# Kernel optimization log

Hardware: AMD Instinct MI355X
Metric: run time of the kernel (lower is better)

Reference implementation:

```python
import jax, jax.numpy as jnp
import numpy as np

P = 7
SCALE = 1.0 / 16.0
PRE_NMS, POST_NMS, NMS_TH, MIN_SIZE = 6000, 300, 0.7, 16.0


def _generate_anchors(base_size=16, ratios=(0.5, 1.0, 2.0), scales=(8, 16, 32)):
    ratios = np.array(ratios, dtype=np.float64)
    scales = np.array(scales, dtype=np.float64)
    base = np.array([0, 0, base_size - 1, base_size - 1], dtype=np.float64)

    def whctrs(a):
        w = a[2] - a[0] + 1
        h = a[3] - a[1] + 1
        return w, h, a[0] + 0.5 * (w - 1), a[1] + 0.5 * (h - 1)

    def mk(ws, hs, xc, yc):
        return np.stack([xc - 0.5 * (ws - 1), yc - 0.5 * (hs - 1),
                         xc + 0.5 * (ws - 1), yc + 0.5 * (hs - 1)], axis=1)

    w, h, xc, yc = whctrs(base)
    size = w * h
    ws = np.round(np.sqrt(size / ratios))
    hs = np.round(ws * ratios)
    ratio_anchors = mk(ws, hs, xc, yc)
    outs = []
    for ra in ratio_anchors:
        w, h, xc, yc = whctrs(ra)
        outs.append(mk(w * scales, h * scales, xc, yc))
    return np.vstack(outs).astype(np.float32)  # [9,4]


def _conv(x, w, b, relu=True):
    y = jax.lax.conv_general_dilated(x, w, (1, 1), 'SAME',
                                     dimension_numbers=('NCHW', 'OIHW', 'NCHW'))
    y = y + b[None, :, None, None]
    return jnp.maximum(y, 0.0) if relu else y


def _maxpool(x):
    return jax.lax.reduce_window(x, -jnp.inf, jax.lax.max,
                                 (1, 1, 2, 2), (1, 1, 2, 2), 'VALID')


def _vgg(x, ws, bs):
    i = 0
    for nb, n in enumerate((2, 2, 3, 3, 3)):
        for _ in range(n):
            x = _conv(x, ws[i], bs[i])
            i += 1
        if nb < 4:
            x = _maxpool(x)
    return x  # conv5_3, stride 16, 512 ch


def _decode(anchors, deltas):
    w = anchors[:, 2] - anchors[:, 0] + 1.0
    h = anchors[:, 3] - anchors[:, 1] + 1.0
    cx = anchors[:, 0] + 0.5 * w
    cy = anchors[:, 1] + 0.5 * h
    pcx = deltas[:, 0] * w + cx
    pcy = deltas[:, 1] * h + cy
    pw = jnp.exp(deltas[:, 2]) * w
    ph = jnp.exp(deltas[:, 3]) * h
    return jnp.stack([pcx - 0.5 * pw, pcy - 0.5 * ph,
                      pcx + 0.5 * pw, pcy + 0.5 * ph], axis=1)


def _nms_keep(boxes, thresh):
    x1, y1, x2, y2 = boxes[:, 0], boxes[:, 1], boxes[:, 2], boxes[:, 3]
    areas = (x2 - x1 + 1.0) * (y2 - y1 + 1.0)
    xx1 = jnp.maximum(x1[:, None], x1[None, :])
    yy1 = jnp.maximum(y1[:, None], y1[None, :])
    xx2 = jnp.minimum(x2[:, None], x2[None, :])
    yy2 = jnp.minimum(y2[:, None], y2[None, :])
    inter = jnp.maximum(xx2 - xx1 + 1.0, 0.0) * jnp.maximum(yy2 - yy1 + 1.0, 0.0)
    iou = inter / (areas[:, None] + areas[None, :] - inter)
    n = boxes.shape[0]
    idx = jnp.arange(n)

    def body(i, keep):
        sup = (iou[i] > thresh) & (idx > i) & keep[i]
        return keep & (~sup)

    return jax.lax.fori_loop(0, n, body, jnp.ones(n, dtype=bool))


def _proposals(prob_fg, bbox_deltas, im_info):
    _, _, H, W = prob_fg.shape
    shift_x = np.arange(W) * 16.0
    shift_y = np.arange(H) * 16.0
    sx, sy = np.meshgrid(shift_x, shift_y)
    shifts = np.stack([sx.ravel(), sy.ravel(), sx.ravel(), sy.ravel()], axis=1).astype(np.float32)
    anchors = jnp.asarray((_generate_anchors()[None, :, :] + shifts[:, None, :]).reshape(-1, 4))
    scores = prob_fg.transpose(0, 2, 3, 1).reshape(-1)
    deltas = bbox_deltas.transpose(0, 2, 3, 1).reshape(-1, 4)
    boxes = _decode(anchors, deltas)
    boxes = jnp.stack([jnp.clip(boxes[:, 0], 0.0, im_info[1] - 1.0),
                       jnp.clip(boxes[:, 1], 0.0, im_info[0] - 1.0),
                       jnp.clip(boxes[:, 2], 0.0, im_info[1] - 1.0),
                       jnp.clip(boxes[:, 3], 0.0, im_info[0] - 1.0)], axis=1)
    ws = boxes[:, 2] - boxes[:, 0] + 1.0
    hs = boxes[:, 3] - boxes[:, 1] + 1.0
    ms = MIN_SIZE * im_info[2]
    scores = jnp.where((ws >= ms) & (hs >= ms), scores, -jnp.inf)
    k = min(PRE_NMS, int(scores.shape[0]))
    top_s, order = jax.lax.top_k(scores, k)
    tb = boxes[order]
    keep = _nms_keep(tb, NMS_TH)
    prio = jnp.where(keep, jnp.arange(k), k)
    sel = jnp.argsort(prio)[:POST_NMS]
    ob = tb[sel]
    rois = jnp.concatenate([jnp.zeros((POST_NMS, 1), ob.dtype), ob], axis=1)
    # original proposal layer runs in numpy -> detached from the graph
    return jax.lax.stop_gradient(rois)


def _roi_pool(feat, rois):
    f = feat[0]  # [C,Hf,Wf]
    C, Hf, Wf = f.shape
    hh = jnp.arange(Hf)
    ww = jnp.arange(Wf)
    pb = jnp.arange(P)

    def one(roi):
        x1 = jnp.round(roi[1] * SCALE).astype(jnp.int32)
        y1 = jnp.round(roi[2] * SCALE).astype(jnp.int32)
        x2 = jnp.round(roi[3] * SCALE).astype(jnp.int32)
        y2 = jnp.round(roi[4] * SCALE).astype(jnp.int32)
        rh = jnp.maximum(y2 - y1 + 1, 1).astype(f.dtype)
        rw = jnp.maximum(x2 - x1 + 1, 1).astype(f.dtype)
        bh = rh / P
        bw = rw / P
        hs_ = jnp.clip(jnp.floor(pb * bh).astype(jnp.int32) + y1, 0, Hf)
        he_ = jnp.clip(jnp.ceil((pb + 1) * bh).astype(jnp.int32) + y1, 0, Hf)
        ws_ = jnp.clip(jnp.floor(pb * bw).astype(jnp.int32) + x1, 0, Wf)
        we_ = jnp.clip(jnp.ceil((pb + 1) * bw).astype(jnp.int32) + x1, 0, Wf)
        mh = (hh[None, :] >= hs_[:, None]) & (hh[None, :] < he_[:, None])  # [P,Hf]
        mw = (ww[None, :] >= ws_[:, None]) & (ww[None, :] < we_[:, None])  # [P,Wf]
        t = jnp.where(mw[:, None, None, :], f[None], -jnp.inf).max(axis=-1)   # [Ppw,C,Hf]
        v = jnp.where(mh[:, None, None, :], t[None], -jnp.inf).max(axis=-1)   # [Pph,Ppw,C]
        v = jnp.where(jnp.isfinite(v), v, 0.0)  # empty bins -> 0
        return jnp.transpose(v, (2, 0, 1))  # [C,P,P]

    return jax.lax.map(one, rois)  # [N,C,P,P]


def _forward(im_data, im_info, vws, vbs, rpn_w, rpn_b, score_w, score_b,
             bbox_w, bbox_b, fc6_w, fc6_b, fc7_w, fc7_b, cls_w, cls_b, breg_w, breg_b):
    x = jnp.transpose(im_data, (0, 3, 1, 2))
    feat = _vgg(x, vws, vbs)
    r = _conv(feat, rpn_w, rpn_b, relu=True)
    score = _conv(r, score_w, score_b, relu=False)  # [1,18,H,W]
    bd = _conv(r, bbox_w, bbox_b, relu=False)       # [1,36,H,W]
    _, _, H, W = score.shape
    # reshape_layer to (1,2,9H,W) + softmax over dim1 == softmax over (1,2,9,H,W) axis 1
    prob = jax.nn.softmax(score.reshape(1, 2, 9, H, W), axis=1).reshape(1, 18, H, W)
    prob_fg = prob[:, 9:, :, :]
    rois = _proposals(prob_fg, bd, im_info)
    pooled = _roi_pool(feat, rois).reshape(POST_NMS, -1)  # [300, 512*7*7]
    h6 = jnp.maximum(pooled @ fc6_w.T + fc6_b, 0.0)
    h7 = jnp.maximum(h6 @ fc7_w.T + fc7_b, 0.0)
    cls_score = h7 @ cls_w.T + cls_b
    cls_prob = jax.nn.softmax(cls_score, axis=-1)
    bbox_pred = h7 @ breg_w.T + breg_b
    return cls_prob, bbox_pred, rois


def setup_inputs() -> dict:
    key = jax.random.key(0)
    ks = iter(jax.random.split(key, 64))
    cfg = [(3, 64), (64, 64), (64, 128), (128, 128), (128, 256), (256, 256), (256, 256),
           (256, 512), (512, 512), (512, 512), (512, 512), (512, 512), (512, 512)]
    inp = {}
    inp['im_data'] = jax.random.uniform(next(ks), (1, 600, 1000, 3), jnp.float32) * 255.0 - 122.0
    inp['im_info'] = jnp.array([600.0, 1000.0, 1.0], jnp.float32)
    for i, (ci, co) in enumerate(cfg, start=1):
        std = float(np.sqrt(2.0 / (ci * 9)))
        inp['vw%d' % i] = jax.random.normal(next(ks), (co, ci, 3, 3), jnp.float32) * std
        inp['vb%d' % i] = jnp.zeros((co,), jnp.float32)
    inp['rpn_w'] = jax.random.normal(next(ks), (512, 512, 3, 3), jnp.float32) * float(np.sqrt(2.0 / (512 * 9)))
    inp['rpn_b'] = jnp.zeros((512,), jnp.float32)
    inp['score_w'] = jax.random.normal(next(ks), (18, 512, 1, 1), jnp.float32) * 0.01
    inp['score_b'] = jnp.zeros((18,), jnp.float32)
    inp['bbox_w'] = jax.random.normal(next(ks), (36, 512, 1, 1), jnp.float32) * 0.01
    inp['bbox_b'] = jnp.zeros((36,), jnp.float32)
    inp['fc6_w'] = jax.random.normal(next(ks), (4096, 512 * 7 * 7), jnp.float32) * 0.005
    inp['fc6_b'] = jnp.zeros((4096,), jnp.float32)
    inp['fc7_w'] = jax.random.normal(next(ks), (4096, 4096), jnp.float32) * 0.01
    inp['fc7_b'] = jnp.zeros((4096,), jnp.float32)
    inp['cls_w'] = jax.random.normal(next(ks), (21, 4096), jnp.float32) * 0.01
    inp['cls_b'] = jnp.zeros((21,), jnp.float32)
    inp['breg_w'] = jax.random.normal(next(ks), (84, 4096), jnp.float32) * 0.001
    inp['breg_b'] = jnp.zeros((84,), jnp.float32)
    return inp


def reference(im_data, im_info, vw1, vb1, vw2, vb2, vw3, vb3, vw4, vb4, vw5, vb5,
              vw6, vb6, vw7, vb7, vw8, vb8, vw9, vb9, vw10, vb10, vw11, vb11,
              vw12, vb12, vw13, vb13, rpn_w, rpn_b, score_w, score_b, bbox_w, bbox_b,
              fc6_w, fc6_b, fc7_w, fc7_b, cls_w, cls_b, breg_w, breg_b):
    vws = [vw1, vw2, vw3, vw4, vw5, vw6, vw7, vw8, vw9, vw10, vw11, vw12, vw13]
    vbs = [vb1, vb2, vb3, vb4, vb5, vb6, vb7, vb8, vb9, vb10, vb11, vb12, vb13]
    return _forward(im_data, im_info, vws, vbs, rpn_w, rpn_b, score_w, score_b,
                    bbox_w, bbox_b, fc6_w, fc6_b, fc7_w, fc7_b, cls_w, cls_b, breg_w, breg_b)
```

## Files before the change

### kernel.cpp

```cpp
#include <hip/hip_runtime.h>
#include <math.h>


#define NPOS 2294
#define FH 37
#define FW 62
#define NANCH 20646
#define NSORT 32768
#define PRE_NMS 6000
#define POST_NMS 300
#define NWORD 94

__device__ const float ANCHORS[9][4] = {
    {-84.f,  -40.f,   99.f,  55.f},
    {-176.f, -88.f,  191.f, 103.f},
    {-360.f, -184.f, 375.f, 199.f},
    {-56.f,  -56.f,   71.f,  71.f},
    {-120.f, -120.f, 135.f, 135.f},
    {-248.f, -248.f, 263.f, 263.f},
    {-36.f,  -80.f,   51.f,  95.f},
    {-80.f,  -168.f,  95.f, 183.f},
    {-168.f, -344.f, 183.f, 359.f},
};

__global__ __launch_bounds__(256) void conv3x3(
    const float* __restrict__ in, const float* __restrict__ w,
    const float* __restrict__ bias, float* __restrict__ out,
    int C, int H, int W, int relu, int nhwc)
{
    __shared__ float patch[10 * 34];
    const int tx = threadIdx.x, ty = threadIdx.y;
    const int tid = ty * 32 + tx;
    const int x0 = blockIdx.x * 32, y0 = blockIdx.y * 8;
    const int k0 = blockIdx.z * 8;
    const size_t HW = (size_t)H * W;

    float acc[8];
#pragma unroll
    for (int i = 0; i < 8; ++i) acc[i] = 0.f;

    for (int c = 0; c < C; ++c) {
        __syncthreads();
#pragma unroll
        for (int l = 0; l < 2; ++l) {
            int idx = tid + l * 256;
            if (idx < 340) {
                int py = idx / 34, px = idx - py * 34;
                int gy = y0 + py - 1, gx = x0 + px - 1;
                float v = 0.f;
                if (gy >= 0 && gy < H && gx >= 0 && gx < W)
                    v = nhwc ? in[((size_t)gy * W + gx) * C + c]
                             : in[(size_t)c * HW + (size_t)gy * W + gx];
                patch[idx] = v;
            }
        }
        __syncthreads();
        float r0 = patch[(ty + 0) * 34 + tx + 0];
        float r1 = patch[(ty + 0) * 34 + tx + 1];
        float r2 = patch[(ty + 0) * 34 + tx + 2];
        float r3 = patch[(ty + 1) * 34 + tx + 0];
        float r4 = patch[(ty + 1) * 34 + tx + 1];
        float r5 = patch[(ty + 1) * 34 + tx + 2];
        float r6 = patch[(ty + 2) * 34 + tx + 0];
        float r7 = patch[(ty + 2) * 34 + tx + 1];
        float r8 = patch[(ty + 2) * 34 + tx + 2];
        const float* wp = w + ((size_t)k0 * C + c) * 9;
#pragma unroll
        for (int ko = 0; ko < 8; ++ko) {
            const float* wk = wp + (size_t)ko * C * 9;
            acc[ko] += wk[0] * r0 + wk[1] * r1 + wk[2] * r2
                     + wk[3] * r3 + wk[4] * r4 + wk[5] * r5
                     + wk[6] * r6 + wk[7] * r7 + wk[8] * r8;
        }
    }

    int gx = x0 + tx, gy = y0 + ty;
    if (gx < W && gy < H) {
#pragma unroll
        for (int ko = 0; ko < 8; ++ko) {
            float v = acc[ko] + bias[k0 + ko];
            if (relu) v = fmaxf(v, 0.f);
            out[(size_t)(k0 + ko) * HW + (size_t)gy * W + gx] = v;
        }
    }
}

__global__ void maxpool2(const float* __restrict__ in, float* __restrict__ out,
                         int C, int H, int W)
{
    int Ho = H >> 1, Wo = W >> 1;
    int total = C * Ho * Wo;
    int idx = blockIdx.x * blockDim.x + threadIdx.x;
    if (idx >= total) return;
    int c = idx / (Ho * Wo);
    int r = idx - c * (Ho * Wo);
    int y = r / Wo, x = r - y * Wo;
    const float* p = in + (size_t)c * H * W + (size_t)(2 * y) * W + 2 * x;
    out[idx] = fmaxf(fmaxf(p[0], p[1]), fmaxf(p[W], p[W + 1]));
}

__global__ void conv1x1(const float* __restrict__ in, const float* __restrict__ w,
                        const float* __restrict__ b, float* __restrict__ out,
                        int C, int P, int K)
{
    int p = blockIdx.x * blockDim.x + threadIdx.x;
    int k = blockIdx.y;
    if (p >= P || k >= K) return;
    const float* wr = w + (size_t)k * C;
    float acc = b[k];
    for (int c = 0; c < C; ++c) acc += wr[c] * in[(size_t)c * P + p];
    out[(size_t)k * P + p] = acc;
}

__global__ void decode_anchors(const float* __restrict__ score,
                               const float* __restrict__ bbox,
                               const float* __restrict__ iminfo,
                               float* __restrict__ boxes,
                               unsigned long long* __restrict__ keys)
{
    int idx = blockIdx.x * blockDim.x + threadIdx.x;
    if (idx >= NSORT) return;
    if (idx >= NANCH) { keys[idx] = ~0ULL; return; }
    int p = idx / 9, a = idx - p * 9;
    int y = p / FW, x = p - y * FW;

    float s0 = score[a * NPOS + p], s1 = score[(9 + a) * NPOS + p];
    float mx = fmaxf(s0, s1);
    float e0 = expf(s0 - mx), e1 = expf(s1 - mx);
    float prob = e1 / (e0 + e1);

    float ax1 = ANCHORS[a][0] + 16.f * x;
    float ay1 = ANCHORS[a][1] + 16.f * y;
    float ax2 = ANCHORS[a][2] + 16.f * x;
    float ay2 = ANCHORS[a][3] + 16.f * y;
    float aw = ax2 - ax1 + 1.f, ah = ay2 - ay1 + 1.f;
    float cx = ax1 + 0.5f * aw, cy = ay1 + 0.5f * ah;

    float d0 = bbox[(4 * a + 0) * NPOS + p];
    float d1 = bbox[(4 * a + 1) * NPOS + p];
    float d2 = bbox[(4 * a + 2) * NPOS + p];
    float d3 = bbox[(4 * a + 3) * NPOS + p];
    float pcx = d0 * aw + cx, pcy = d1 * ah + cy;
    float pw = expf(d2) * aw, ph = expf(d3) * ah;

    float imh = iminfo[0], imw = iminfo[1], sc = iminfo[2];
    float x1 = fminf(fmaxf(pcx - 0.5f * pw, 0.f), imw - 1.f);
    float y1 = fminf(fmaxf(pcy - 0.5f * ph, 0.f), imh - 1.f);
    float x2 = fminf(fmaxf(pcx + 0.5f * pw, 0.f), imw - 1.f);
    float y2 = fminf(fmaxf(pcy + 0.5f * ph, 0.f), imh - 1.f);
    boxes[idx * 4 + 0] = x1; boxes[idx * 4 + 1] = y1;
    boxes[idx * 4 + 2] = x2; boxes[idx * 4 + 3] = y2;

    float wsz = x2 - x1 + 1.f, hsz = y2 - y1 + 1.f;
    float ms = 16.f * sc;
    float s = (wsz >= ms && hsz >= ms) ? prob : -INFINITY;
    unsigned u = __float_as_uint(s);
    u = (u & 0x80000000u) ? ~u : (u | 0x80000000u);
    unsigned k32 = ~u;
    keys[idx] = ((unsigned long long)k32 << 32) | (unsigned)idx;
}

__global__ void bitonic_step(unsigned long long* __restrict__ keys, int j, int k)
{
    int i = blockIdx.x * blockDim.x + threadIdx.x;
    int ixj = i ^ j;
    if (ixj > i && ixj < NSORT) {
        unsigned long long a = keys[i], b = keys[ixj];
        bool up = ((i & k) == 0);
        if ((a > b) == up) { keys[i] = b; keys[ixj] = a; }
    }
}

__global__ void gather_top(const unsigned long long* __restrict__ keys,
                           const float* __restrict__ boxes, float* __restrict__ tb)
{
    int r = blockIdx.x * blockDim.x + threadIdx.x;
    if (r >= PRE_NMS) return;
    int idx = (int)(keys[r] & 0xffffffffULL);
    ((float4*)tb)[r] = ((const float4*)boxes)[idx];
}

__global__ __launch_bounds__(128) void iou_sup(const float* __restrict__ tb,
                                               unsigned long long* __restrict__ sup)
{
    int i = blockIdx.x;
    int wj = threadIdx.x;
    if (wj >= NWORD) return;
    float4 bi = ((const float4*)tb)[i];
    float ai = (bi.z - bi.x + 1.f) * (bi.w - bi.y + 1.f);
    unsigned long long m = 0;
    int jbase = wj * 64;
    for (int b = 0; b < 64; ++b) {
        int j = jbase + b;
        if (j <= i || j >= PRE_NMS) continue;
        float4 bj = ((const float4*)tb)[j];
        float xx1 = fmaxf(bi.x, bj.x), yy1 = fmaxf(bi.y, bj.y);
        float xx2 = fminf(bi.z, bj.z), yy2 = fminf(bi.w, bj.w);
        float iw = fmaxf(xx2 - xx1 + 1.f, 0.f), ih = fmaxf(yy2 - yy1 + 1.f, 0.f);
        float inter = iw * ih;
        float aj = (bj.z - bj.x + 1.f) * (bj.w - bj.y + 1.f);
        float iou = inter / (ai + aj - inter);
        if (iou > 0.7f) m |= (1ULL << b);
    }
    sup[(size_t)i * NWORD + wj] = m;
}

__global__ __launch_bounds__(128) void nms_seq(const unsigned long long* __restrict__ sup,
                                               unsigned long long* __restrict__ keepg)
{
    __shared__ unsigned long long keep[NWORD];
    int t = threadIdx.x;
    if (t < NWORD) keep[t] = ~0ULL;
    __syncthreads();
    for (int i = 0; i < PRE_NMS; ++i) {
        bool k = (keep[i >> 6] >> (i & 63)) & 1ULL;
        __syncthreads();
        if (k && t < NWORD) keep[t] &= ~sup[(size_t)i * NWORD + t];
        __syncthreads();
    }
    if (t < NWORD) keepg[t] = keep[t];
}

__global__ void select_rois(const unsigned long long* __restrict__ keepg,
                            const float* __restrict__ tb,
                            float* __restrict__ rois, float* __restrict__ out_rois)
{
    if (threadIdx.x != 0 || blockIdx.x != 0) return;
    int cnt = 0;
    for (int pass = 0; pass < 2 && cnt < POST_NMS; ++pass) {
        for (int i = 0; i < PRE_NMS && cnt < POST_NMS; ++i) {
            bool k = (keepg[i >> 6] >> (i & 63)) & 1ULL;
            if ((pass == 0) == k) {
                float v0 = 0.f;
                float v1 = tb[i * 4 + 0], v2 = tb[i * 4 + 1];
                float v3 = tb[i * 4 + 2], v4 = tb[i * 4 + 3];
                rois[cnt * 5 + 0] = v0; rois[cnt * 5 + 1] = v1; rois[cnt * 5 + 2] = v2;
                rois[cnt * 5 + 3] = v3; rois[cnt * 5 + 4] = v4;
                out_rois[cnt * 5 + 0] = v0; out_rois[cnt * 5 + 1] = v1; out_rois[cnt * 5 + 2] = v2;
                out_rois[cnt * 5 + 3] = v3; out_rois[cnt * 5 + 4] = v4;
                ++cnt;
            }
        }
    }
}

__global__ __launch_bounds__(256) void roi_pool(const float* __restrict__ feat,
                                                const float* __restrict__ rois,
                                                float* __restrict__ pooled)
{
    int b = blockIdx.x;
    const float* r = rois + b * 5;
    int x1 = (int)rintf(r[1] * 0.0625f);
    int y1 = (int)rintf(r[2] * 0.0625f);
    int x2 = (int)rintf(r[3] * 0.0625f);
    int y2 = (int)rintf(r[4] * 0.0625f);
    float bh = (float)max(y2 - y1 + 1, 1) / 7.f;
    float bw = (float)max(x2 - x1 + 1, 1) / 7.f;
    for (int o = threadIdx.x; o < 512 * 49; o += 256) {
        int c = o / 49, rem = o - c * 49;
        int ph = rem / 7, pw = rem - ph * 7;
        int hs = min(max((int)floorf(ph * bh) + y1, 0), FH);
        int he = min(max((int)ceilf((ph + 1) * bh) + y1, 0), FH);
        int wst = min(max((int)floorf(pw * bw) + x1, 0), FW);
        int wen = min(max((int)ceilf((pw + 1) * bw) + x1, 0), FW);
        float m = -INFINITY;
        for (int yy = hs; yy < he; ++yy)
            for (int xx = wst; xx < wen; ++xx)
                m = fmaxf(m, feat[c * NPOS + yy * FW + xx]);
        pooled[(size_t)b * 25088 + o] = (he > hs && wen > wst) ? m : 0.f;
    }
}

__global__ __launch_bounds__(256) void gemm_nt(const float* __restrict__ A,
                                               const float* __restrict__ Wt,
                                               const float* __restrict__ bias,
                                               float* __restrict__ out,
                                               int M, int N, int K, int relu)
{
    __shared__ float Ws[32 * 260];
    __shared__ float As[32 * 20];
    int t = threadIdx.x;
    int n0 = blockIdx.x * 256, m0 = blockIdx.y * 16;
    int tnn = t & 63, tmm = t >> 6;
    float acc[4][4];
#pragma unroll
    for (int i = 0; i < 4; ++i)
#pragma unroll
        for (int j = 0; j < 4; ++j) acc[i][j] = 0.f;

    for (int k0 = 0; k0 < K; k0 += 32) {
        __syncthreads();
        {
            const float4* wr = (const float4*)(Wt + (size_t)(n0 + t) * K + k0);
#pragma unroll
            for (int q = 0; q < 8; ++q) {
                float4 v = wr[q];
                Ws[(4 * q + 0) * 260 + t] = v.x;
                Ws[(4 * q + 1) * 260 + t] = v.y;
                Ws[(4 * q + 2) * 260 + t] = v.z;
                Ws[(4 * q + 3) * 260 + t] = v.w;
            }
        }
        if (t < 128) {
            int m = t >> 3, q = t & 7;
            float4 v = make_float4(0.f, 0.f, 0.f, 0.f);
            if (m0 + m < M) v = *(const float4*)(A + (size_t)(m0 + m) * K + k0 + 4 * q);
            As[(4 * q + 0) * 20 + m] = v.x;
            As[(4 * q + 1) * 20 + m] = v.y;
            As[(4 * q + 2) * 20 + m] = v.z;
            As[(4 * q + 3) * 20 + m] = v.w;
        }
        __syncthreads();
#pragma unroll 8
        for (int kk = 0; kk < 32; ++kk) {
            float4 wv = *(const float4*)&Ws[kk * 260 + tnn * 4];
            float4 av = *(const float4*)&As[kk * 20 + tmm * 4];
            acc[0][0] += av.x * wv.x; acc[0][1] += av.x * wv.y;
            acc[0][2] += av.x * wv.z; acc[0][3] += av.x * wv.w;
            acc[1][0] += av.y * wv.x; acc[1][1] += av.y * wv.y;
            acc[1][2] += av.y * wv.z; acc[1][3] += av.y * wv.w;
            acc[2][0] += av.z * wv.x; acc[2][1] += av.z * wv.y;
            acc[2][2] += av.z * wv.z; acc[2][3] += av.z * wv.w;
            acc[3][0] += av.w * wv.x; acc[3][1] += av.w * wv.y;
            acc[3][2] += av.w * wv.z; acc[3][3] += av.w * wv.w;
        }
    }
    int n = n0 + tnn * 4;
    float4 bv = *(const float4*)(bias + n);
#pragma unroll
    for (int i = 0; i < 4; ++i) {
        int m = m0 + tmm * 4 + i;
        if (m < M) {
            float4 o;
            o.x = acc[i][0] + bv.x; o.y = acc[i][1] + bv.y;
            o.z = acc[i][2] + bv.z; o.w = acc[i][3] + bv.w;
            if (relu) {
                o.x = fmaxf(o.x, 0.f); o.y = fmaxf(o.y, 0.f);
                o.z = fmaxf(o.z, 0.f); o.w = fmaxf(o.w, 0.f);
            }
            *(float4*)(out + (size_t)m * N + n) = o;
        }
    }
}

__global__ void fc_small(const float* __restrict__ A, const float* __restrict__ Wt,
                         const float* __restrict__ bias, float* __restrict__ out,
                         int N, int K)
{
    int m = blockIdx.x, n = threadIdx.x;
    if (n >= N) return;
    const float4* a = (const float4*)(A + (size_t)m * K);
    const float4* w = (const float4*)(Wt + (size_t)n * K);
    float acc = bias[n];
    for (int q = 0; q < K / 4; ++q) {
        float4 av = a[q], wv = w[q];
        acc += av.x * wv.x + av.y * wv.y + av.z * wv.z + av.w * wv.w;
    }
    out[(size_t)m * N + n] = acc;
}

__global__ void softmax21(const float* __restrict__ in, float* __restrict__ out)
{
    int r = blockIdx.x * blockDim.x + threadIdx.x;
    if (r >= POST_NMS) return;
    const float* x = in + r * 21;
    float m = x[0];
    for (int j = 1; j < 21; ++j) m = fmaxf(m, x[j]);
    float e[21], s = 0.f;
    for (int j = 0; j < 21; ++j) { e[j] = expf(x[j] - m); s += e[j]; }
    float inv = 1.f / s;
    for (int j = 0; j < 21; ++j) out[r * 21 + j] = e[j] * inv;
}

extern "C" void kernel_launch(void* const* d_in, const int* in_sizes, int n_in,
                              void* d_out, int out_size, void* d_ws, size_t ws_size,
                              hipStream_t stream)
{
    const float* im_data = (const float*)d_in[0];
    const float* im_info = (const float*)d_in[1];
    const float* vw[13]; const float* vb[13];
    for (int i = 0; i < 13; ++i) { vw[i] = (const float*)d_in[2 + 2 * i]; vb[i] = (const float*)d_in[3 + 2 * i]; }
    const float* rpn_w   = (const float*)d_in[28];
    const float* rpn_b   = (const float*)d_in[29];
    const float* score_w = (const float*)d_in[30];
    const float* score_b = (const float*)d_in[31];
    const float* bbox_w  = (const float*)d_in[32];
    const float* bbox_b  = (const float*)d_in[33];
    const float* fc6_w   = (const float*)d_in[34];
    const float* fc6_b   = (const float*)d_in[35];
    const float* fc7_w   = (const float*)d_in[36];
    const float* fc7_b   = (const float*)d_in[37];
    const float* cls_w   = (const float*)d_in[38];
    const float* cls_b   = (const float*)d_in[39];
    const float* breg_w  = (const float*)d_in[40];
    const float* breg_b  = (const float*)d_in[41];

    float* ws = (float*)d_ws;
    const size_t oA    = 0;
    const size_t oB    = 38400000;
    const size_t oF    = 76800000;
    const size_t oRPN  = oF    + 1174528;
    const size_t oSC   = oRPN  + 1174528;
    const size_t oBB   = oSC   + 41292;
    const size_t oBOX  = oBB   + 82584;
    const size_t oKEY  = oBOX  + 82584;
    const size_t oTB   = oKEY  + 65536;
    const size_t oSUP  = oTB   + 24000;
    const size_t oKEEP = oSUP  + 1128000;
    const size_t oROI  = oKEEP + 256;
    const size_t oPOOL = oROI  + 1536;
    const size_t oH6   = oPOOL + 7526400;
    const size_t oH7   = oH6   + 1228800;
    const size_t oCLS  = oH7   + 1228800;

    float* bufA = ws + oA;
    float* bufB = ws + oB;
    float* feat = ws + oF;
    float* rpn  = ws + oRPN;
    float* scr  = ws + oSC;
    float* bbx  = ws + oBB;
    float* boxes = ws + oBOX;
    unsigned long long* keys = (unsigned long long*)(ws + oKEY);
    float* tb = ws + oTB;
    unsigned long long* sup = (unsigned long long*)(ws + oSUP);
    unsigned long long* keepg = (unsigned long long*)(ws + oKEEP);
    float* rois = ws + oROI;
    float* pooled = ws + oPOOL;
    float* h6 = ws + oH6;
    float* h7 = ws + oH7;
    float* clsb = ws + oCLS;

    float* out = (float*)d_out;
    float* out_bbox = out + 6300;
    float* out_rois = out + 31500;

    dim3 cblk(32, 8);
    auto conv = [&](const float* in, const float* w, const float* b, float* o,
                    int C, int H, int W, int K, int relu, int nhwc) {
        dim3 grid((W + 31) / 32, (H + 7) / 8, K / 8);
        conv3x3<<<grid, cblk, 0, stream>>>(in, w, b, o, C, H, W, relu, nhwc);
    };
    auto pool = [&](const float* in, float* o, int C, int H, int W) {
        int total = C * (H / 2) * (W / 2);
        maxpool2<<<(total + 255) / 256, 256, 0, stream>>>(in, o, C, H, W);
    };

    conv(im_data, vw[0], vb[0], bufA, 3, 600, 1000, 64, 1, 1);
    conv(bufA, vw[1], vb[1], bufB, 64, 600, 1000, 64, 1, 0);
    pool(bufB, bufA, 64, 600, 1000);
    conv(bufA, vw[2], vb[2], bufB, 64, 300, 500, 128, 1, 0);
    conv(bufB, vw[3], vb[3], bufA, 128, 300, 500, 128, 1, 0);
    pool(bufA, bufB, 128, 300, 500);
    conv(bufB, vw[4], vb[4], bufA, 128, 150, 250, 256, 1, 0);
    conv(bufA, vw[5], vb[5], bufB, 256, 150, 250, 256, 1, 0);
    conv(bufB, vw[6], vb[6], bufA, 256, 150, 250, 256, 1, 0);
    pool(bufA, bufB, 256, 150, 250);
    conv(bufB, vw[7], vb[7], bufA, 256, 75, 125, 512, 1, 0);
    conv(bufA, vw[8], vb[8], bufB, 512, 75, 125, 512, 1, 0);
    conv(bufB, vw[9], vb[9], bufA, 512, 75, 125, 512, 1, 0);
    pool(bufA, bufB, 512, 75, 125);
    conv(bufB, vw[10], vb[10], bufA, 512, FH, FW, 512, 1, 0);
    conv(bufA, vw[11], vb[11], bufB, 512, FH, FW, 512, 1, 0);
    conv(bufB, vw[12], vb[12], feat, 512, FH, FW, 512, 1, 0);

    conv(feat, rpn_w, rpn_b, rpn, 512, FH, FW, 512, 1, 0);
    {
        dim3 g((NPOS + 255) / 256, 18);
        conv1x1<<<g, 256, 0, stream>>>(rpn, score_w, score_b, scr, 512, NPOS, 18);
    }
    {
        dim3 g((NPOS + 255) / 256, 36);
        conv1x1<<<g, 256, 0, stream>>>(rpn, bbox_w, bbox_b, bbx, 512, NPOS, 36);
    }

    decode_anchors<<<NSORT / 256, 256, 0, stream>>>(scr, bbx, im_info, boxes, keys);
    for (int k = 2; k <= NSORT; k <<= 1)
        for (int j = k >> 1; j > 0; j >>= 1)
            bitonic_step<<<NSORT / 256, 256, 0, stream>>>(keys, j, k);
    gather_top<<<(PRE_NMS + 255) / 256, 256, 0, stream>>>(keys, boxes, tb);
    iou_sup<<<PRE_NMS, 128, 0, stream>>>(tb, sup);
    nms_seq<<<1, 128, 0, stream>>>(sup, keepg);
    select_rois<<<1, 64, 0, stream>>>(keepg, tb, rois, out_rois);

    roi_pool<<<POST_NMS, 256, 0, stream>>>(feat, rois, pooled);
    {
        dim3 g(4096 / 256, (POST_NMS + 15) / 16);
        gemm_nt<<<g, 256, 0, stream>>>(pooled, fc6_w, fc6_b, h6, POST_NMS, 4096, 25088, 1);
        gemm_nt<<<g, 256, 0, stream>>>(h6, fc7_w, fc7_b, h7, POST_NMS, 4096, 4096, 1);
    }
    fc_small<<<POST_NMS, 96, 0, stream>>>(h7, cls_w, cls_b, clsb, 21, 4096);
    fc_small<<<POST_NMS, 96, 0, stream>>>(h7, breg_w, breg_b, out_bbox, 84, 4096);
    softmax21<<<(POST_NMS + 255) / 256, 256, 0, stream>>>(clsb, out);
    (void)in_sizes; (void)n_in; (void)out_size; (void)ws_size;
}
```

Measured before the change: 17.50 ms.

## Batch conv channels, shared-memory bitonic sort, wave NMS, split-K FC GEMMs

Result: slower. 20.00 ms (+14.3%).

```diff
diff --git a/kernel.cpp b/kernel.cpp
--- a/kernel.cpp
+++ b/kernel.cpp
@@ -10,6 +10,7 @@
 #define PRE_NMS 6000
 #define POST_NMS 300
 #define NWORD 94
+#define GS 8
 
 __device__ const float ANCHORS[9][4] = {
     {-84.f,  -40.f,   99.f,  55.f},
@@ -28,7 +29,7 @@
     const float* __restrict__ bias, float* __restrict__ out,
     int C, int H, int W, int relu, int nhwc)
 {
-    __shared__ float patch[10 * 34];
+    __shared__ float patch[4][10][34];
     const int tx = threadIdx.x, ty = threadIdx.y;
     const int tid = ty * 32 + tx;
     const int x0 = blockIdx.x * 32, y0 = blockIdx.y * 8;
@@ -39,38 +40,49 @@
 #pragma unroll
     for (int i = 0; i < 8; ++i) acc[i] = 0.f;
 
-    for (int c = 0; c < C; ++c) {
+    for (int c0 = 0; c0 < C; c0 += 4) {
+        const int nc = (C - c0 >= 4) ? 4 : (C - c0);
         __syncthreads();
-#pragma unroll
-        for (int l = 0; l < 2; ++l) {
-            int idx = tid + l * 256;
-            if (idx < 340) {
-                int py = idx / 34, px = idx - py * 34;
-                int gy = y0 + py - 1, gx = x0 + px - 1;
-                float v = 0.f;
-                if (gy >= 0 && gy < H && gx >= 0 && gx < W)
-                    v = nhwc ? in[((size_t)gy * W + gx) * C + c]
-                             : in[(size_t)c * HW + (size_t)gy * W + gx];
-                patch[idx] = v;
+        for (int idx = tid; idx < nc * 340; idx += 256) {
+            int cc = idx / 340, rr = idx - cc * 340;
+            int py = rr / 34, px = rr - py * 34;
+            int gy = y0 + py - 1, gx = x0 + px - 1;
+            float v = 0.f;
+            if (gy >= 0 && gy < H && gx >= 0 && gx < W)
+                v = nhwc ? in[((size_t)gy * W + gx) * C + (c0 + cc)]
+                         : in[(size_t)(c0 + cc) * HW + (size_t)gy * W + gx];
+            patch[cc][py][px] = v;
+        }
+        __syncthreads();
+        if (nc == 4) {
+#pragma unroll
+            for (int cc = 0; cc < 4; ++cc) {
+                float r0 = patch[cc][ty][tx],     r1 = patch[cc][ty][tx + 1],     r2 = patch[cc][ty][tx + 2];
+                float r3 = patch[cc][ty + 1][tx], r4 = patch[cc][ty + 1][tx + 1], r5 = patch[cc][ty + 1][tx + 2];
+                float r6 = patch[cc][ty + 2][tx], r7 = patch[cc][ty + 2][tx + 1], r8 = patch[cc][ty + 2][tx + 2];
+                const float* wp = w + ((size_t)k0 * C + (c0 + cc)) * 9;
+#pragma unroll
+                for (int ko = 0; ko < 8; ++ko) {
+                    const float* wk = wp + (size_t)ko * C * 9;
+                    acc[ko] += wk[0] * r0 + wk[1] * r1 + wk[2] * r2
+                             + wk[3] * r3 + wk[4] * r4 + wk[5] * r5
+                             + wk[6] * r6 + wk[7] * r7 + wk[8] * r8;
+                }
             }
-        }
-        __syncthreads();
-        float r0 = patch[(ty + 0) * 34 + tx + 0];
-        float r1 = patch[(ty + 0) * 34 + tx + 1];
-        float r2 = patch[(ty + 0) * 34 + tx + 2];
-        float r3 = patch[(ty + 1) * 34 + tx + 0];
-        float r4 = patch[(ty + 1) * 34 + tx + 1];
-        float r5 = patch[(ty + 1) * 34 + tx + 2];
-        float r6 = patch[(ty + 2) * 34 + tx + 0];
-        float r7 = patch[(ty + 2) * 34 + tx + 1];
-        float r8 = patch[(ty + 2) * 34 + tx + 2];
-        const float* wp = w + ((size_t)k0 * C + c) * 9;
-#pragma unroll
-        for (int ko = 0; ko < 8; ++ko) {
-            const float* wk = wp + (size_t)ko * C * 9;
-            acc[ko] += wk[0] * r0 + wk[1] * r1 + wk[2] * r2
-                     + wk[3] * r3 + wk[4] * r4 + wk[5] * r5
-                     + wk[6] * r6 + wk[7] * r7 + wk[8] * r8;
+        } else {
+            for (int cc = 0; cc < nc; ++cc) {
+                float r0 = patch[cc][ty][tx],     r1 = patch[cc][ty][tx + 1],     r2 = patch[cc][ty][tx + 2];
+                float r3 = patch[cc][ty + 1][tx], r4 = patch[cc][ty + 1][tx + 1], r5 = patch[cc][ty + 1][tx + 2];
+                float r6 = patch[cc][ty + 2][tx], r7 = patch[cc][ty + 2][tx + 1], r8 = patch[cc][ty + 2][tx + 2];
+                const float* wp = w + ((size_t)k0 * C + (c0 + cc)) * 9;
+#pragma unroll
+                for (int ko = 0; ko < 8; ++ko) {
+                    const float* wk = wp + (size_t)ko * C * 9;
+                    acc[ko] += wk[0] * r0 + wk[1] * r1 + wk[2] * r2
+                             + wk[3] * r3 + wk[4] * r4 + wk[5] * r5
+                             + wk[6] * r6 + wk[7] * r7 + wk[8] * r8;
+                }
+            }
         }
     }
 
@@ -169,6 +181,40 @@
         bool up = ((i & k) == 0);
         if ((a > b) == up) { keys[i] = b; keys[ixj] = a; }
     }
+}
+
+__global__ __launch_bounds__(1024) void bitonic_local(unsigned long long* __restrict__ keys,
+                                                      int mode, int kbig)
+{
+    __shared__ unsigned long long s[2048];
+    const int t = threadIdx.x;
+    const int base = blockIdx.x * 2048;
+    s[t] = keys[base + t];
+    s[t + 1024] = keys[base + t + 1024];
+    __syncthreads();
+    if (mode == 0) {
+        for (int k = 2; k <= 2048; k <<= 1) {
+            for (int j = k >> 1; j > 0; j >>= 1) {
+                int i = ((t & ~(j - 1)) << 1) | (t & (j - 1));
+                int ixj = i + j;
+                bool up = (((base + i) & k) == 0);
+                unsigned long long a = s[i], b = s[ixj];
+                if ((a > b) == up) { s[i] = b; s[ixj] = a; }
+                __syncthreads();
+            }
+        }
+    } else {
+        for (int j = 1024; j > 0; j >>= 1) {
+            int i = ((t & ~(j - 1)) << 1) | (t & (j - 1));
+            int ixj = i + j;
+            bool up = (((base + i) & kbig) == 0);
+            unsigned long long a = s[i], b = s[ixj];
+            if ((a > b) == up) { s[i] = b; s[ixj] = a; }
+            __syncthreads();
+        }
+    }
+    keys[base + t] = s[t];
+    keys[base + t + 1024] = s[t + 1024];
 }
 
 __global__ void gather_top(const unsigned long long* __restrict__ keys,
@@ -205,41 +251,65 @@
     sup[(size_t)i * NWORD + wj] = m;
 }
 
-__global__ __launch_bounds__(128) void nms_seq(const unsigned long long* __restrict__ sup,
-                                               unsigned long long* __restrict__ keepg)
-{
-    __shared__ unsigned long long keep[NWORD];
-    int t = threadIdx.x;
-    if (t < NWORD) keep[t] = ~0ULL;
+__global__ void nms_wave(const unsigned long long* __restrict__ sup,
+                         unsigned long long* __restrict__ keepg)
+{
+    const int l = threadIdx.x;
+    const bool hi = (64 + l < NWORD);
+    unsigned long long w0 = ~0ULL;
+    unsigned long long w1 = hi ? ~0ULL : 0ULL;
+
+    unsigned long long a0, b0, a1, b1, a2, b2, a3, b3, a4, b4, a5, b5, a6, b6, a7, b7;
+#define LOADROW(A, B, r) do { \
+        A = sup[(size_t)(r) * NWORD + l]; \
+        B = hi ? sup[(size_t)(r) * NWORD + 64 + l] : 0ULL; } while (0)
+    LOADROW(a0, b0, 0); LOADROW(a1, b1, 1); LOADROW(a2, b2, 2); LOADROW(a3, b3, 3);
+    LOADROW(a4, b4, 4); LOADROW(a5, b5, 5); LOADROW(a6, b6, 6); LOADROW(a7, b7, 7);
+
+    for (int g = 0; g < PRE_NMS; g += 8) {
+#define STEP(A, B, ii) do { \
+        int i = g + (ii); \
+        int wi = i >> 6; \
+        unsigned long long kw = (wi < 64) ? __shfl(w0, wi) : __shfl(w1, wi - 64); \
+        if ((kw >> (i & 63)) & 1ULL) { w0 &= ~(A); w1 &= ~(B); } \
+        int nr = i + 8; \
+        if (nr < PRE_NMS) LOADROW(A, B, nr); } while (0)
+        STEP(a0, b0, 0); STEP(a1, b1, 1); STEP(a2, b2, 2); STEP(a3, b3, 3);
+        STEP(a4, b4, 4); STEP(a5, b5, 5); STEP(a6, b6, 6); STEP(a7, b7, 7);
+#undef STEP
+    }
+#undef LOADROW
+    if (l == 29) w1 &= (1ULL << 48) - 1ULL;
+    keepg[l] = w0;
+    if (hi) keepg[64 + l] = w1;
+}
+
+__global__ __launch_bounds__(128) void select_rois(
+    const unsigned long long* __restrict__ keepg,
+    const float* __restrict__ tb,
+    float* __restrict__ rois, float* __restrict__ out_rois)
+{
+    __shared__ int wbase[NWORD + 1];
+    const int t = threadIdx.x;
+    if (t == 0) {
+        int s = 0;
+        for (int w = 0; w < NWORD; ++w) { wbase[w] = s; s += __popcll(keepg[w]); }
+        wbase[NWORD] = s;
+    }
     __syncthreads();
-    for (int i = 0; i < PRE_NMS; ++i) {
-        bool k = (keep[i >> 6] >> (i & 63)) & 1ULL;
-        __syncthreads();
-        if (k && t < NWORD) keep[t] &= ~sup[(size_t)i * NWORD + t];
-        __syncthreads();
-    }
-    if (t < NWORD) keepg[t] = keep[t];
-}
-
-__global__ void select_rois(const unsigned long long* __restrict__ keepg,
-                            const float* __restrict__ tb,
-                            float* __restrict__ rois, float* __restrict__ out_rois)
-{
-    if (threadIdx.x != 0 || blockIdx.x != 0) return;
-    int cnt = 0;
-    for (int pass = 0; pass < 2 && cnt < POST_NMS; ++pass) {
-        for (int i = 0; i < PRE_NMS && cnt < POST_NMS; ++i) {
-            bool k = (keepg[i >> 6] >> (i & 63)) & 1ULL;
-            if ((pass == 0) == k) {
-                float v0 = 0.f;
-                float v1 = tb[i * 4 + 0], v2 = tb[i * 4 + 1];
-                float v3 = tb[i * 4 + 2], v4 = tb[i * 4 + 3];
-                rois[cnt * 5 + 0] = v0; rois[cnt * 5 + 1] = v1; rois[cnt * 5 + 2] = v2;
-                rois[cnt * 5 + 3] = v3; rois[cnt * 5 + 4] = v4;
-                out_rois[cnt * 5 + 0] = v0; out_rois[cnt * 5 + 1] = v1; out_rois[cnt * 5 + 2] = v2;
-                out_rois[cnt * 5 + 3] = v3; out_rois[cnt * 5 + 4] = v4;
-                ++cnt;
-            }
+    const int K = wbase[NWORD];
+    for (int i = t; i < PRE_NMS; i += 128) {
+        unsigned long long wd = keepg[i >> 6];
+        int bit = i & 63;
+        bool kept = (wd >> bit) & 1ULL;
+        int before = wbase[i >> 6] + __popcll(wd & ((1ULL << bit) - 1ULL));
+        int rank = kept ? before : (K + i - before);
+        if (rank < POST_NMS) {
+            float4 bx = ((const float4*)tb)[i];
+            float* r1 = rois + rank * 5;
+            float* r2 = out_rois + rank * 5;
+            r1[0] = 0.f; r1[1] = bx.x; r1[2] = bx.y; r1[3] = bx.z; r1[4] = bx.w;
+            r2[0] = 0.f; r2[1] = bx.x; r2[2] = bx.y; r2[3] = bx.z; r2[4] = bx.w;
         }
     }
 }
@@ -271,76 +341,93 @@
     }
 }
 
-__global__ __launch_bounds__(256) void gemm_nt(const float* __restrict__ A,
-                                               const float* __restrict__ Wt,
-                                               const float* __restrict__ bias,
-                                               float* __restrict__ out,
-                                               int M, int N, int K, int relu)
-{
-    __shared__ float Ws[32 * 260];
-    __shared__ float As[32 * 20];
-    int t = threadIdx.x;
-    int n0 = blockIdx.x * 256, m0 = blockIdx.y * 16;
-    int tnn = t & 63, tmm = t >> 6;
-    float acc[4][4];
-#pragma unroll
-    for (int i = 0; i < 4; ++i)
-#pragma unroll
-        for (int j = 0; j < 4; ++j) acc[i][j] = 0.f;
-
-    for (int k0 = 0; k0 < K; k0 += 32) {
+__global__ __launch_bounds__(256) void gemm_splitk(
+    const float* __restrict__ A, const float* __restrict__ Wt,
+    float* __restrict__ P, int M, int N, int K)
+{
+    __shared__ float As[32][64];
+    __shared__ float Ws[32][256];
+    const int t = threadIdx.x;
+    const int n0 = blockIdx.x * 256;
+    const int m0 = blockIdx.y * 64;
+    const int Kc = K / GS;
+    const int kbeg = blockIdx.z * Kc;
+    const int tn = t & 31, tm = t >> 5;
+
+    float acc[8][8];
+#pragma unroll
+    for (int i = 0; i < 8; ++i)
+#pragma unroll
+        for (int j = 0; j < 8; ++j) acc[i][j] = 0.f;
+
+    for (int k0 = kbeg; k0 < kbeg + Kc; k0 += 32) {
         __syncthreads();
         {
             const float4* wr = (const float4*)(Wt + (size_t)(n0 + t) * K + k0);
 #pragma unroll
             for (int q = 0; q < 8; ++q) {
                 float4 v = wr[q];
-                Ws[(4 * q + 0) * 260 + t] = v.x;
-                Ws[(4 * q + 1) * 260 + t] = v.y;
-                Ws[(4 * q + 2) * 260 + t] = v.z;
-                Ws[(4 * q + 3) * 260 + t] = v.w;
+                Ws[4 * q + 0][t] = v.x; Ws[4 * q + 1][t] = v.y;
+                Ws[4 * q + 2][t] = v.z; Ws[4 * q + 3][t] = v.w;
             }
         }
-        if (t < 128) {
-            int m = t >> 3, q = t & 7;
+#pragma unroll
+        for (int u = 0; u < 2; ++u) {
+            int task = t + u * 256;
+            int m = task >> 3, q = task & 7;
             float4 v = make_float4(0.f, 0.f, 0.f, 0.f);
             if (m0 + m < M) v = *(const float4*)(A + (size_t)(m0 + m) * K + k0 + 4 * q);
-            As[(4 * q + 0) * 20 + m] = v.x;
-            As[(4 * q + 1) * 20 + m] = v.y;
-            As[(4 * q + 2) * 20 + m] = v.z;
-            As[(4 * q + 3) * 20 + m] = v.w;
+            As[4 * q + 0][m] = v.x; As[4 * q + 1][m] = v.y;
+            As[4 * q + 2][m] = v.z; As[4 * q + 3][m] = v.w;
         }
         __syncthreads();
-#pragma unroll 8
+#pragma unroll 4
         for (int kk = 0; kk < 32; ++kk) {
-            float4 wv = *(const float4*)&Ws[kk * 260 + tnn * 4];
-            float4 av = *(const float4*)&As[kk * 20 + tmm * 4];
-            acc[0][0] += av.x * wv.x; acc[0][1] += av.x * wv.y;
-            acc[0][2] += av.x * wv.z; acc[0][3] += av.x * wv.w;
-            acc[1][0] += av.y * wv.x; acc[1][1] += av.y * wv.y;
-            acc[1][2] += av.y * wv.z; acc[1][3] += av.y * wv.w;
-            acc[2][0] += av.z * wv.x; acc[2][1] += av.z * wv.y;
-            acc[2][2] += av.z * wv.z; acc[2][3] += av.z * wv.w;
-            acc[3][0] += av.w * wv.x; acc[3][1] += av.w * wv.y;
-            acc[3][2] += av.w * wv.z; acc[3][3] += av.w * wv.w;
-        }
-    }
-    int n = n0 + tnn * 4;
-    float4 bv = *(const float4*)(bias + n);
-#pragma unroll
-    for (int i = 0; i < 4; ++i) {
-        int m = m0 + tmm * 4 + i;
+            float4 av0 = *(const float4*)&As[kk][tm * 8];
+            float4 av1 = *(const float4*)&As[kk][tm * 8 + 4];
+            float a[8] = {av0.x, av0.y, av0.z, av0.w, av1.x, av1.y, av1.z, av1.w};
+            float wv[8];
+#pragma unroll
+            for (int j = 0; j < 8; ++j) wv[j] = Ws[kk][tn + (j << 5)];
+#pragma unroll
+            for (int i = 0; i < 8; ++i)
+#pragma unroll
+                for (int j = 0; j < 8; ++j) acc[i][j] += a[i] * wv[j];
+        }
+    }
+
+    float* Pp = P + (size_t)blockIdx.z * M * N;
+#pragma unroll
+    for (int i = 0; i < 8; ++i) {
+        int m = m0 + tm * 8 + i;
         if (m < M) {
-            float4 o;
-            o.x = acc[i][0] + bv.x; o.y = acc[i][1] + bv.y;
-            o.z = acc[i][2] + bv.z; o.w = acc[i][3] + bv.w;
-            if (relu) {
-                o.x = fmaxf(o.x, 0.f); o.y = fmaxf(o.y, 0.f);
-                o.z = fmaxf(o.z, 0.f); o.w = fmaxf(o.w, 0.f);
-            }
-            *(float4*)(out + (size_t)m * N + n) = o;
-        }
-    }
+            float* row = Pp + (size_t)m * N + n0 + tn;
+#pragma unroll
+            for (int j = 0; j < 8; ++j) row[j << 5] = acc[i][j];
+        }
+    }
+}
+
+__global__ void splitk_reduce(const float* __restrict__ P, const float* __restrict__ bias,
+                              float* __restrict__ out, int M, int N, int relu)
+{
+    int idx = blockIdx.x * 256 + threadIdx.x;
+    int total = (M * N) >> 2;
+    if (idx >= total) return;
+    float4 s = ((const float4*)P)[idx];
+#pragma unroll
+    for (int g = 1; g < GS; ++g) {
+        float4 v = ((const float4*)P)[(size_t)g * total + idx];
+        s.x += v.x; s.y += v.y; s.z += v.z; s.w += v.w;
+    }
+    int n = (idx << 2) % N;
+    float4 b = *(const float4*)(bias + n);
+    s.x += b.x; s.y += b.y; s.z += b.z; s.w += b.w;
+    if (relu) {
+        s.x = fmaxf(s.x, 0.f); s.y = fmaxf(s.y, 0.f);
+        s.z = fmaxf(s.z, 0.f); s.w = fmaxf(s.w, 0.f);
+    }
+    ((float4*)out)[idx] = s;
 }
 
 __global__ void fc_small(const float* __restrict__ A, const float* __restrict__ Wt,
@@ -474,19 +561,26 @@
     }
 
     decode_anchors<<<NSORT / 256, 256, 0, stream>>>(scr, bbx, im_info, boxes, keys);
-    for (int k = 2; k <= NSORT; k <<= 1)
-        for (int j = k >> 1; j > 0; j >>= 1)
+    bitonic_local<<<NSORT / 2048, 1024, 0, stream>>>(keys, 0, 0);
+    for (int k = 4096; k <= NSORT; k <<= 1) {
+        for (int j = k >> 1; j >= 2048; j >>= 1)
             bitonic_step<<<NSORT / 256, 256, 0, stream>>>(keys, j, k);
+        bitonic_local<<<NSORT / 2048, 1024, 0, stream>>>(keys, 1, k);
+    }
     gather_top<<<(PRE_NMS + 255) / 256, 256, 0, stream>>>(keys, boxes, tb);
     iou_sup<<<PRE_NMS, 128, 0, stream>>>(tb, sup);
-    nms_seq<<<1, 128, 0, stream>>>(sup, keepg);
-    select_rois<<<1, 64, 0, stream>>>(keepg, tb, rois, out_rois);
+    nms_wave<<<1, 64, 0, stream>>>(sup, keepg);
+    select_rois<<<1, 128, 0, stream>>>(keepg, tb, rois, out_rois);
 
     roi_pool<<<POST_NMS, 256, 0, stream>>>(feat, rois, pooled);
     {
-        dim3 g(4096 / 256, (POST_NMS + 15) / 16);
-        gemm_nt<<<g, 256, 0, stream>>>(pooled, fc6_w, fc6_b, h6, POST_NMS, 4096, 25088, 1);
-        gemm_nt<<<g, 256, 0, stream>>>(h6, fc7_w, fc7_b, h7, POST_NMS, 4096, 4096, 1);
+        float* Pbuf = bufA;
+        dim3 g6(4096 / 256, (POST_NMS + 63) / 64, GS);
+        int rblocks = (POST_NMS * 4096 / 4 + 255) / 256;
+        gemm_splitk<<<g6, 256, 0, stream>>>(pooled, fc6_w, Pbuf, POST_NMS, 4096, 25088);
+        splitk_reduce<<<rblocks, 256, 0, stream>>>(Pbuf, fc6_b, h6, POST_NMS, 4096, 1);
+        gemm_splitk<<<g6, 256, 0, stream>>>(h6, fc7_w, Pbuf, POST_NMS, 4096, 4096);
+        splitk_reduce<<<rblocks, 256, 0, stream>>>(Pbuf, fc7_b, h7, POST_NMS, 4096, 1);
     }
     fc_small<<<POST_NMS, 96, 0, stream>>>(h7, cls_w, cls_b, clsb, 21, 4096);
     fc_small<<<POST_NMS, 96, 0, stream>>>(h7, breg_w, breg_b, out_bbox, 84, 4096);
```
